# Kernel optimization log

Hardware: AMD Instinct MI355X
Metric: run time of the kernel (lower is better)

## Reference

```python
import jax, jax.numpy as jnp
import numpy as np

N_NODES = 50000
N_EDGES = 800000
IN_DIM, FEAT_DIM, HID_DIM, OUT_DIM = 512, 256, 256, 128


def _glorot(key, shape):
    fan_in = shape[-1]
    bound = 1.0 / np.sqrt(fan_in)
    return jax.random.uniform(key, shape, jnp.float32, -bound, bound)


def setup_inputs() -> dict:
    key = jax.random.key(0)
    ks = jax.random.split(key, 12)
    x = jax.random.normal(ks[0], (N_NODES, IN_DIM), jnp.float32)
    edge_index = jax.random.randint(ks[1], (2, N_EDGES), 0, N_NODES, jnp.int64)
    return {
        "x": x,
        "edge_index": edge_index,
        # feature_pre MLP
        "W_pre": _glorot(ks[2], (FEAT_DIM, IN_DIM)),
        "b_pre": jnp.zeros((FEAT_DIM,), jnp.float32),
        "W_pre2": _glorot(ks[3], (HID_DIM, FEAT_DIM)),
        "b_pre2": jnp.zeros((HID_DIM,), jnp.float32),
        # conv_first: SAGEConv(hidden, hidden); lin_l (neighbors, with bias), lin_r (root, no bias)
        "Wl1": _glorot(ks[4], (HID_DIM, HID_DIM)),
        "bl1": jnp.zeros((HID_DIM,), jnp.float32),
        "Wr1": _glorot(ks[5], (HID_DIM, HID_DIM)),
        # conv_out: SAGEConv(hidden, output)
        "Wl2": _glorot(ks[6], (OUT_DIM, HID_DIM)),
        "bl2": jnp.zeros((OUT_DIM,), jnp.float32),
        "Wr2": _glorot(ks[7], (OUT_DIM, HID_DIM)),
    }


def sage_conv(x, src, dst, Wl, bl, Wr):
    # mean-aggregate source features at destination nodes, then linear + root linear
    n = x.shape[0]
    msg = x[src]                                               # [E, D]
    agg = jax.ops.segment_sum(msg, dst, num_segments=n)        # [N, D]
    cnt = jax.ops.segment_sum(jnp.ones((src.shape[0],), x.dtype), dst, num_segments=n)
    mean = agg / jnp.maximum(cnt, 1.0)[:, None]
    return mean @ Wl.T + bl + x @ Wr.T


def reference(x, edge_index, W_pre, b_pre, W_pre2, b_pre2, Wl1, bl1, Wr1, Wl2, bl2, Wr2):
    src, dst = edge_index[0], edge_index[1]
    h = x @ W_pre.T + b_pre
    h = h @ W_pre2.T + b_pre2
    h = jax.nn.relu(sage_conv(h, src, dst, Wl1, bl1, Wr1))
    # dropout is identity in eval mode; layer_num=2 -> no hidden convs
    h = sage_conv(h, src, dst, Wl2, bl2, Wr2)
    # F.normalize(p=2, dim=-1), eps=1e-12
    norm = jnp.maximum(jnp.linalg.norm(h, axis=-1, keepdims=True), 1e-12)
    return h / norm
```

## Files before the change

kernel.cpp:

```cpp
#include <hip/hip_runtime.h>
#include <hip/hip_bf16.h>


typedef __attribute__((ext_vector_type(4))) float f32x4;
typedef __attribute__((ext_vector_type(8))) short s8v;

__device__ __forceinline__ float bf2f(unsigned short u) {
  union { unsigned int i; float f; } v; v.i = ((unsigned int)u) << 16; return v.f;
}
__device__ __forceinline__ unsigned short f2bf(float f) {
  unsigned int u = __builtin_bit_cast(unsigned int, f);
  u += 0x7fffu + ((u >> 16) & 1u);
  return (unsigned short)(u >> 16);
}

__global__ __launch_bounds__(256) void zero_int_kernel(int* __restrict__ p, int n) {
  int i = blockIdx.x * blockDim.x + threadIdx.x;
  const int stride = gridDim.x * blockDim.x;
  for (; i < n; i += stride) p[i] = 0;
}

__global__ __launch_bounds__(256) void count_kernel(const int* __restrict__ dst,
                                                    int* __restrict__ cnt, int E) {
  const int e = blockIdx.x * blockDim.x + threadIdx.x;
  if (e < E) atomicAdd(&cnt[dst[e]], 1);
}

__global__ __launch_bounds__(256) void scan_pass1(const int* __restrict__ cnt,
                                                  int* __restrict__ bsum, int M) {
  __shared__ int red[256];
  const int t = threadIdx.x;
  const int i = blockIdx.x * 256 + t;
  red[t] = (i < M) ? cnt[i] : 0;
  __syncthreads();
  for (int off = 128; off > 0; off >>= 1) {
    if (t < off) red[t] += red[t + off];
    __syncthreads();
  }
  if (t == 0) bsum[blockIdx.x] = red[0];
}

__global__ __launch_bounds__(256) void scan_pass2(const int* __restrict__ bsum,
    int* __restrict__ boff, int* __restrict__ rowptr, int nb, int M, int E) {
  __shared__ int buf[256];
  const int t = threadIdx.x;
  const int v = (t < nb) ? bsum[t] : 0;
  buf[t] = v;
  __syncthreads();
  for (int off = 1; off < 256; off <<= 1) {
    const int add = (t >= off) ? buf[t - off] : 0;
    __syncthreads();
    buf[t] += add;
    __syncthreads();
  }
  if (t < nb) boff[t] = buf[t] - v;
  if (t == 0) rowptr[M] = E;
}

__global__ __launch_bounds__(256) void scan_pass3(int* __restrict__ cnt,
    const int* __restrict__ boff, int* __restrict__ rowptr, int M) {
  __shared__ int buf[256];
  const int t = threadIdx.x;
  const int i = blockIdx.x * 256 + t;
  const int v = (i < M) ? cnt[i] : 0;
  buf[t] = v;
  __syncthreads();
  for (int off = 1; off < 256; off <<= 1) {
    const int add = (t >= off) ? buf[t - off] : 0;
    __syncthreads();
    buf[t] += add;
    __syncthreads();
  }
  if (i < M) {
    rowptr[i] = buf[t] - v + boff[blockIdx.x];
    cnt[i] = 0;
  }
}

__global__ __launch_bounds__(256) void fill_kernel(const int* __restrict__ src,
    const int* __restrict__ dst, const int* __restrict__ rowptr,
    int* __restrict__ cursor, unsigned short* __restrict__ eidx, int E) {
  const int e = blockIdx.x * blockDim.x + threadIdx.x;
  if (e >= E) return;
  const int d = dst[e];
  const int pos = rowptr[d] + atomicAdd(&cursor[d], 1);
  eidx[pos] = (unsigned short)src[e];
}

__global__ __launch_bounds__(256) void cvt_x_kernel(const float* __restrict__ x,
    unsigned short* __restrict__ xb, int n) {
  int i = (blockIdx.x * 256 + threadIdx.x) * 8;
  const int stride = gridDim.x * 256 * 8;
  for (; i < n; i += stride) {
    const float4 f0 = *(const float4*)(x + i);
    const float4 f1 = *(const float4*)(x + i + 4);
    s8v p;
    p[0] = (short)f2bf(f0.x); p[1] = (short)f2bf(f0.y);
    p[2] = (short)f2bf(f0.z); p[3] = (short)f2bf(f0.w);
    p[4] = (short)f2bf(f1.x); p[5] = (short)f2bf(f1.y);
    p[6] = (short)f2bf(f1.z); p[7] = (short)f2bf(f1.w);
    *(s8v*)(xb + i) = p;
  }
}

__global__ __launch_bounds__(256) void prep_kernel(const float* __restrict__ Wp,
    const float* __restrict__ Wp2, const float* __restrict__ bp,
    const float* __restrict__ bp2, const float* __restrict__ Wl1,
    const float* __restrict__ Wr1, const float* __restrict__ Wl2,
    const float* __restrict__ Wr2, unsigned short* __restrict__ Wc,
    float* __restrict__ bc, unsigned short* __restrict__ Bc1,
    unsigned short* __restrict__ Bc2) {
  const int b = blockIdx.x, t = threadIdx.x;
  if (b < 256) {
    __shared__ float wrow[256];
    wrow[t] = Wp2[b * 256 + t];
    __syncthreads();
    float a0 = 0.f, a1 = 0.f;
    for (int m = 0; m < 256; ++m) {
      const float w = wrow[m];
      a0 = fmaf(w, Wp[m * 512 + t], a0);
      a1 = fmaf(w, Wp[m * 512 + 256 + t], a1);
    }
    Wc[b * 512 + t] = f2bf(a0);
    Wc[b * 512 + 256 + t] = f2bf(a1);
  } else if (b == 256) {
    float s = 0.f;
    for (int m = 0; m < 256; ++m) s = fmaf(Wp2[t * 256 + m], bp[m], s);
    bc[t] = s + bp2[t];
  } else if (b < 769) {
    const int idx = (b - 257) * 256 + t;
    const int o = idx >> 9, k = idx & 511;
    const float v = (k < 256) ? Wl1[o * 256 + k] : Wr1[o * 256 + (k - 256)];
    Bc1[idx] = f2bf(v);
  } else {
    const int idx = (b - 769) * 256 + t;
    const int r = idx >> 8, k = idx & 255;
    const float v = (r < 128) ? Wl2[r * 256 + k] : Wr2[(r - 128) * 256 + k];
    Bc2[idx] = f2bf(v);
  }
}

template <int K, int ASTRIDE, int CSTRIDE, int CBASE, bool BIAS_EN, bool RELU_EN>
__global__ __launch_bounds__(256) void mfma_gemm(
    const unsigned short* __restrict__ Ap, const unsigned short* __restrict__ Bp,
    const float* __restrict__ bias, unsigned short* __restrict__ Cp, int M, int nwg) {
  constexpr int NT = K / 32;
  constexpr int BUF = 16384;
  __shared__ __align__(16) char smem[3 * BUF];

  const int xcd = blockIdx.x & 7, bidx = blockIdx.x >> 3;
  const int q = nwg >> 3, r = nwg & 7;
  const int wg = (xcd < r ? xcd * (q + 1) : r * (q + 1) + (xcd - r) * q) + bidx;
  const int bm = (wg >> 1) * 128;
  const int bn = (wg & 1) * 128;

  const int t = threadIdx.x, w = t >> 6, l = t & 63;
  const int wr = (w >> 1) * 64, wc = (w & 1) * 64;
  const int lane15 = l & 15, half = l >> 4;

  const int sr = t >> 2, sp = t & 3;
  const int ar0 = min(bm + sr, M - 1);
  const int ar1 = min(bm + 64 + sr, M - 1);
  const int sl0 = sp ^ ((sr >> 1) & 3);
  const int sl1 = sp ^ (((64 + sr) >> 1) & 3);
  const unsigned short* apb0 = Ap + (size_t)ar0 * ASTRIDE + sl0 * 8;
  const unsigned short* apb1 = Ap + (size_t)ar1 * ASTRIDE + sl1 * 8;
  const unsigned short* bpb0 = Bp + (size_t)(bn + sr) * K + sl0 * 8;
  const unsigned short* bpb1 = Bp + (size_t)(bn + 64 + sr) * K + sl1 * 8;

  f32x4 acc[4][4];
#pragma unroll
  for (int i = 0; i < 4; ++i)
#pragma unroll
    for (int j = 0; j < 4; ++j) acc[i][j] = f32x4{0.f, 0.f, 0.f, 0.f};

  auto stage = [&](int bufOff, int k0) {
    __builtin_amdgcn_global_load_lds((const unsigned int*)(apb0 + k0),
        (unsigned int*)(smem + bufOff + w * 1024), 16, 0, 0);
    __builtin_amdgcn_global_load_lds((const unsigned int*)(apb1 + k0),
        (unsigned int*)(smem + bufOff + 4096 + w * 1024), 16, 0, 0);
    __builtin_amdgcn_global_load_lds((const unsigned int*)(bpb0 + k0),
        (unsigned int*)(smem + bufOff + 8192 + w * 1024), 16, 0, 0);
    __builtin_amdgcn_global_load_lds((const unsigned int*)(bpb1 + k0),
        (unsigned int*)(smem + bufOff + 12288 + w * 1024), 16, 0, 0);
  };
  auto compute = [&](int bufOff) {
    const char* Ab = smem + bufOff;
    const char* Bb = Ab + 8192;
    s8v af[4], bv[4];
#pragma unroll
    for (int ms = 0; ms < 4; ++ms) {
      const int rr = wr + ms * 16 + lane15;
      af[ms] = *(const s8v*)(Ab + rr * 64 + ((half ^ ((rr >> 1) & 3)) << 4));
    }
#pragma unroll
    for (int ns = 0; ns < 4; ++ns) {
      const int rr = wc + ns * 16 + lane15;
      bv[ns] = *(const s8v*)(Bb + rr * 64 + ((half ^ ((rr >> 1) & 3)) << 4));
    }
#pragma unroll
    for (int ms = 0; ms < 4; ++ms)
#pragma unroll
      for (int ns = 0; ns < 4; ++ns)
        acc[ms][ns] =
            __builtin_amdgcn_mfma_f32_16x16x32_bf16(af[ms], bv[ns], acc[ms][ns], 0, 0, 0);
  };

  stage(0, 0);
  stage(BUF, 32);

  int offC = 0, offI = 2 * BUF;
#pragma unroll 1
  for (int tt = 0; tt < NT - 1; ++tt) {
    asm volatile("s_waitcnt vmcnt(4)" ::: "memory");
    __builtin_amdgcn_sched_barrier(0);
    __builtin_amdgcn_s_barrier();
    if (tt + 2 < NT) stage(offI, (tt + 2) * 32);
    compute(offC);
    offC = (offC == 2 * BUF) ? 0 : offC + BUF;
    offI = (offI == 2 * BUF) ? 0 : offI + BUF;
  }
  asm volatile("s_waitcnt vmcnt(0)" ::: "memory");
  __builtin_amdgcn_sched_barrier(0);
  __builtin_amdgcn_s_barrier();
  compute(offC);

  float bias_l[4];
  if (BIAS_EN) {
#pragma unroll
    for (int ns = 0; ns < 4; ++ns) bias_l[ns] = bias[bn + wc + ns * 16 + lane15];
  }
  constexpr int PITCH = 288;
#pragma unroll
  for (int pp = 0; pp < 2; ++pp) {
    __syncthreads();
#pragma unroll
    for (int mi = 0; mi < 2; ++mi) {
      const int ms = 2 * pp + mi;
      const int lrow0 = (wr >> 1) + (mi << 4) + half * 4;
#pragma unroll
      for (int ns = 0; ns < 4; ++ns) {
        f32x4 v = acc[ms][ns];
        if (BIAS_EN) {
#pragma unroll
          for (int rg = 0; rg < 4; ++rg) v[rg] += bias_l[ns];
        }
        if (RELU_EN) {
#pragma unroll
          for (int rg = 0; rg < 4; ++rg) v[rg] = fmaxf(v[rg], 0.f);
        }
        const int colb = (wc + ns * 16 + lane15) * 2;
#pragma unroll
        for (int rg = 0; rg < 4; ++rg)
          *(unsigned short*)(smem + (lrow0 + rg) * PITCH + colb) = f2bf(v[rg]);
      }
    }
    __syncthreads();
#pragma unroll
    for (int jj = 0; jj < 4; ++jj) {
      const int lr = jj * 16 + (t >> 4);
      const int wrg = (lr >= 32) ? 64 : 0;
      const int msg = 2 * pp + ((lr >> 4) & 1);
      const int grow = bm + wrg + msg * 16 + (lr & 15);
      if (grow < M) {
        const s8v val = *(const s8v*)(smem + lr * PITCH + lane15 * 16);
        *(s8v*)(Cp + (size_t)grow * CSTRIDE + CBASE + bn + lane15 * 8) = val;
      }
    }
  }
}

__global__ __launch_bounds__(256) void gather_mean256_kernel(
    unsigned short* __restrict__ Acat, const int* __restrict__ rowptr,
    const unsigned short* __restrict__ eidx, int M) {
  const int node = blockIdx.x * 4 + (threadIdx.x >> 6);
  if (node >= M) return;
  const int lane = threadIdx.x & 63;
  const int c4 = lane * 4;
  const int beg = rowptr[node], end = rowptr[node + 1];
  float a0 = 0.f, a1 = 0.f, a2 = 0.f, a3 = 0.f;
  int j = beg;
  for (; j + 3 < end; j += 4) {
    const size_t s0 = eidx[j], s1 = eidx[j + 1], s2 = eidx[j + 2], s3 = eidx[j + 3];
    const ushort4 v0 = *(const ushort4*)(Acat + s0 * 512 + 256 + c4);
    const ushort4 v1 = *(const ushort4*)(Acat + s1 * 512 + 256 + c4);
    const ushort4 v2 = *(const ushort4*)(Acat + s2 * 512 + 256 + c4);
    const ushort4 v3 = *(const ushort4*)(Acat + s3 * 512 + 256 + c4);
    a0 += (bf2f(v0.x) + bf2f(v1.x)) + (bf2f(v2.x) + bf2f(v3.x));
    a1 += (bf2f(v0.y) + bf2f(v1.y)) + (bf2f(v2.y) + bf2f(v3.y));
    a2 += (bf2f(v0.z) + bf2f(v1.z)) + (bf2f(v2.z) + bf2f(v3.z));
    a3 += (bf2f(v0.w) + bf2f(v1.w)) + (bf2f(v2.w) + bf2f(v3.w));
  }
  for (; j < end; ++j) {
    const size_t s0 = eidx[j];
    const ushort4 v0 = *(const ushort4*)(Acat + s0 * 512 + 256 + c4);
    a0 += bf2f(v0.x); a1 += bf2f(v0.y); a2 += bf2f(v0.z); a3 += bf2f(v0.w);
  }
  const float inv = 1.0f / fmaxf((float)(end - beg), 1.0f);
  ushort4 o;
  o.x = f2bf(a0 * inv); o.y = f2bf(a1 * inv);
  o.z = f2bf(a2 * inv); o.w = f2bf(a3 * inv);
  *(ushort4*)(Acat + (size_t)node * 512 + c4) = o;
}

__global__ __launch_bounds__(256) void gather_finalize_kernel(
    const unsigned short* __restrict__ Acat, const int* __restrict__ rowptr,
    const unsigned short* __restrict__ eidx, const float* __restrict__ bl2,
    float* __restrict__ out, int M) {
  const int node = blockIdx.x * 4 + (threadIdx.x >> 6);
  if (node >= M) return;
  const int lane = threadIdx.x & 63;
  const int c2 = lane * 2;
  const int beg = rowptr[node], end = rowptr[node + 1];
  float ax = 0.f, ay = 0.f;
  int j = beg;
  for (; j + 3 < end; j += 4) {
    const size_t s0 = eidx[j], s1 = eidx[j + 1], s2 = eidx[j + 2], s3 = eidx[j + 3];
    const ushort2 v0 = *(const ushort2*)(Acat + s0 * 512 + 256 + c2);
    const ushort2 v1 = *(const ushort2*)(Acat + s1 * 512 + 256 + c2);
    const ushort2 v2 = *(const ushort2*)(Acat + s2 * 512 + 256 + c2);
    const ushort2 v3 = *(const ushort2*)(Acat + s3 * 512 + 256 + c2);
    ax += (bf2f(v0.x) + bf2f(v1.x)) + (bf2f(v2.x) + bf2f(v3.x));
    ay += (bf2f(v0.y) + bf2f(v1.y)) + (bf2f(v2.y) + bf2f(v3.y));
  }
  for (; j < end; ++j) {
    const size_t s0 = eidx[j];
    const ushort2 v0 = *(const ushort2*)(Acat + s0 * 512 + 256 + c2);
    ax += bf2f(v0.x); ay += bf2f(v0.y);
  }
  const float inv = 1.0f / fmaxf((float)(end - beg), 1.0f);
  const ushort2 rr = *(const ushort2*)(Acat + (size_t)node * 512 + 384 + c2);
  const float2 b = *(const float2*)&bl2[c2];
  const float vx = fmaf(ax, inv, b.x) + bf2f(rr.x);
  const float vy = fmaf(ay, inv, b.y) + bf2f(rr.y);
  float ss = vx * vx + vy * vy;
#pragma unroll
  for (int off = 32; off > 0; off >>= 1) ss += __shfl_xor(ss, off);
  const float rn = 1.0f / fmaxf(sqrtf(ss), 1e-12f);
  *(float2*)&out[(size_t)node * 128 + c2] = make_float2(vx * rn, vy * rn);
}

extern "C" void kernel_launch(void* const* d_in, const int* in_sizes, int n_in,
                              void* d_out, int out_size, void* d_ws, size_t ws_size,
                              hipStream_t stream) {
  const float* x      = (const float*)d_in[0];
  const int*   ei     = (const int*)d_in[1];
  const float* W_pre  = (const float*)d_in[2];
  const float* b_pre  = (const float*)d_in[3];
  const float* W_pre2 = (const float*)d_in[4];
  const float* b_pre2 = (const float*)d_in[5];
  const float* Wl1    = (const float*)d_in[6];
  const float* bl1    = (const float*)d_in[7];
  const float* Wr1    = (const float*)d_in[8];
  const float* Wl2    = (const float*)d_in[9];
  const float* bl2    = (const float*)d_in[10];
  const float* Wr2    = (const float*)d_in[11];
  float* out = (float*)d_out;

  const int M = in_sizes[0] / 512;
  const int E = in_sizes[1] / 2;
  const int* src = ei;
  const int* dst = ei + E;

  char* p = (char*)d_ws;
  unsigned short* Acat = (unsigned short*)p; p += (size_t)M * 512 * 2;
  unsigned short* H3   = (unsigned short*)p; p += (size_t)M * 256 * 2;
  unsigned short* xb   = (unsigned short*)p; p += (size_t)M * 512 * 2;
  unsigned short* Wc   = (unsigned short*)p; p += 256 * 512 * 2;
  unsigned short* Bc1  = (unsigned short*)p; p += 256 * 512 * 2;
  unsigned short* Bc2  = (unsigned short*)p; p += 256 * 256 * 2;
  float* bc   = (float*)p; p += 256 * 4;
  int* rowptr = (int*)p;   p += (size_t)(M + 1) * 4;
  int* cnt    = (int*)p;   p += (size_t)M * 4;
  int* bsum   = (int*)p;   p += 256 * 4;
  int* boff   = (int*)p;   p += 256 * 4;
  unsigned short* eidx = (unsigned short*)p;

  const int eblk = (E + 255) / 256;
  const int nb   = (M + 255) / 256;
  const int nwg  = ((M + 127) / 128) * 2;
  const int nblk = (M + 3) / 4;

  cvt_x_kernel<<<2048, 256, 0, stream>>>(x, xb, M * 512);

  zero_int_kernel<<<256, 256, 0, stream>>>(cnt, M);
  count_kernel<<<eblk, 256, 0, stream>>>(dst, cnt, E);
  scan_pass1<<<nb, 256, 0, stream>>>(cnt, bsum, M);
  scan_pass2<<<1, 256, 0, stream>>>(bsum, boff, rowptr, nb, M, E);
  scan_pass3<<<nb, 256, 0, stream>>>(cnt, boff, rowptr, M);
  fill_kernel<<<eblk, 256, 0, stream>>>(src, dst, rowptr, cnt, eidx, E);

  prep_kernel<<<1025, 256, 0, stream>>>(W_pre, W_pre2, b_pre, b_pre2,
                                        Wl1, Wr1, Wl2, Wr2, Wc, bc, Bc1, Bc2);

  mfma_gemm<512, 512, 512, 256, true, false>
      <<<nwg, 256, 0, stream>>>(xb, Wc, bc, Acat, M, nwg);
  gather_mean256_kernel<<<nblk, 256, 0, stream>>>(Acat, rowptr, eidx, M);
  mfma_gemm<512, 512, 256, 0, true, true>
      <<<nwg, 256, 0, stream>>>(Acat, Bc1, bl1, H3, M, nwg);
  mfma_gemm<256, 256, 512, 256, false, false>
      <<<nwg, 256, 0, stream>>>(H3, Bc2, nullptr, Acat, M, nwg);
  gather_finalize_kernel<<<nblk, 256, 0, stream>>>(Acat, rowptr, eidx, bl2, out, M);
}
```

Measured before the change: 288.0 us.

## Fuse fp32-to-bf16 conversion of input into first GEMM's A-tile staging

Removes the separate conversion kernel and its bf16 workspace buffer; the first GEMM now loads fp32 rows of x into registers, converts them to bf16 and writes them into swizzled LDS. The B operand still uses direct global-to-LDS loads. This is meant to cut the extra memory round trip and one kernel launch. In exchange the GEMM reads twice as many bytes for A, including redundant reads across the two column-tile workgroups, and it adds register pressure and VALU conversion work inside the pipelined loop.

```diff
diff --git a/kernel.cpp b/kernel.cpp
--- a/kernel.cpp
+++ b/kernel.cpp
@@ -85,22 +85,6 @@
   const int d = dst[e];
   const int pos = rowptr[d] + atomicAdd(&cursor[d], 1);
   eidx[pos] = (unsigned short)src[e];
-}
-
-__global__ __launch_bounds__(256) void cvt_x_kernel(const float* __restrict__ x,
-    unsigned short* __restrict__ xb, int n) {
-  int i = (blockIdx.x * 256 + threadIdx.x) * 8;
-  const int stride = gridDim.x * 256 * 8;
-  for (; i < n; i += stride) {
-    const float4 f0 = *(const float4*)(x + i);
-    const float4 f1 = *(const float4*)(x + i + 4);
-    s8v p;
-    p[0] = (short)f2bf(f0.x); p[1] = (short)f2bf(f0.y);
-    p[2] = (short)f2bf(f0.z); p[3] = (short)f2bf(f0.w);
-    p[4] = (short)f2bf(f1.x); p[5] = (short)f2bf(f1.y);
-    p[6] = (short)f2bf(f1.z); p[7] = (short)f2bf(f1.w);
-    *(s8v*)(xb + i) = p;
-  }
 }
 
 __global__ __launch_bounds__(256) void prep_kernel(const float* __restrict__ Wp,
@@ -140,10 +124,10 @@
   }
 }
 
-template <int K, int ASTRIDE, int CSTRIDE, int CBASE, bool BIAS_EN, bool RELU_EN>
-__global__ __launch_bounds__(256) void mfma_gemm(
-    const unsigned short* __restrict__ Ap, const unsigned short* __restrict__ Bp,
-    const float* __restrict__ bias, unsigned short* __restrict__ Cp, int M, int nwg) {
+template <int K, int ASTRIDE, int CSTRIDE, int CBASE, bool BIAS_EN, bool RELU_EN, bool A_FP32>
+__global__ __launch_bounds__(256) void mfma_gemm(const void* __restrict__ Ap,
+    const unsigned short* __restrict__ Bp, const float* __restrict__ bias,
+    unsigned short* __restrict__ Cp, int M, int nwg) {
   constexpr int NT = K / 32;
   constexpr int BUF = 16384;
   __shared__ __align__(16) char smem[3 * BUF];
@@ -159,22 +143,26 @@
   const int lane15 = l & 15, half = l >> 4;
 
   const int sr = t >> 2, sp = t & 3;
-  const int ar0 = min(bm + sr, M - 1);
-  const int ar1 = min(bm + 64 + sr, M - 1);
   const int sl0 = sp ^ ((sr >> 1) & 3);
   const int sl1 = sp ^ (((64 + sr) >> 1) & 3);
-  const unsigned short* apb0 = Ap + (size_t)ar0 * ASTRIDE + sl0 * 8;
-  const unsigned short* apb1 = Ap + (size_t)ar1 * ASTRIDE + sl1 * 8;
+  const unsigned short* Abf = (const unsigned short*)Ap;
+  const unsigned short* apb0 = Abf + (size_t)min(bm + sr, M - 1) * ASTRIDE + sl0 * 8;
+  const unsigned short* apb1 = Abf + (size_t)min(bm + 64 + sr, M - 1) * ASTRIDE + sl1 * 8;
   const unsigned short* bpb0 = Bp + (size_t)(bn + sr) * K + sl0 * 8;
   const unsigned short* bpb1 = Bp + (size_t)(bn + 64 + sr) * K + sl1 * 8;
 
+  const int fr = t >> 1, fh = t & 1;
+  const float* Afp = (const float*)Ap + (size_t)min(bm + fr, M - 1) * ASTRIDE + fh * 16;
+  const int fs0 = (2 * fh + 0) ^ ((fr >> 1) & 3);
+  const int fs1 = (2 * fh + 1) ^ ((fr >> 1) & 3);
+
   f32x4 acc[4][4];
 #pragma unroll
   for (int i = 0; i < 4; ++i)
 #pragma unroll
     for (int j = 0; j < 4; ++j) acc[i][j] = f32x4{0.f, 0.f, 0.f, 0.f};
 
-  auto stage = [&](int bufOff, int k0) {
+  auto stageAll = [&](int bufOff, int k0) {
     __builtin_amdgcn_global_load_lds((const unsigned int*)(apb0 + k0),
         (unsigned int*)(smem + bufOff + w * 1024), 16, 0, 0);
     __builtin_amdgcn_global_load_lds((const unsigned int*)(apb1 + k0),
@@ -184,6 +172,31 @@
     __builtin_amdgcn_global_load_lds((const unsigned int*)(bpb1 + k0),
         (unsigned int*)(smem + bufOff + 12288 + w * 1024), 16, 0, 0);
   };
+  auto stageB2 = [&](int bufOff, int k0) {
+    __builtin_amdgcn_global_load_lds((const unsigned int*)(bpb0 + k0),
+        (unsigned int*)(smem + bufOff + 8192 + w * 1024), 16, 0, 0);
+    __builtin_amdgcn_global_load_lds((const unsigned int*)(bpb1 + k0),
+        (unsigned int*)(smem + bufOff + 12288 + w * 1024), 16, 0, 0);
+  };
+  auto loadA = [&](int k0, float4* ar) {
+    ar[0] = *(const float4*)(Afp + k0 + 0);
+    ar[1] = *(const float4*)(Afp + k0 + 4);
+    ar[2] = *(const float4*)(Afp + k0 + 8);
+    ar[3] = *(const float4*)(Afp + k0 + 12);
+  };
+  auto writeA = [&](int bufOff, const float4* ar) {
+    s8v p0, p1;
+    p0[0] = (short)f2bf(ar[0].x); p0[1] = (short)f2bf(ar[0].y);
+    p0[2] = (short)f2bf(ar[0].z); p0[3] = (short)f2bf(ar[0].w);
+    p0[4] = (short)f2bf(ar[1].x); p0[5] = (short)f2bf(ar[1].y);
+    p0[6] = (short)f2bf(ar[1].z); p0[7] = (short)f2bf(ar[1].w);
+    p1[0] = (short)f2bf(ar[2].x); p1[1] = (short)f2bf(ar[2].y);
+    p1[2] = (short)f2bf(ar[2].z); p1[3] = (short)f2bf(ar[2].w);
+    p1[4] = (short)f2bf(ar[3].x); p1[5] = (short)f2bf(ar[3].y);
+    p1[6] = (short)f2bf(ar[3].z); p1[7] = (short)f2bf(ar[3].w);
+    *(s8v*)(smem + bufOff + fr * 64 + fs0 * 16) = p0;
+    *(s8v*)(smem + bufOff + fr * 64 + fs1 * 16) = p1;
+  };
   auto compute = [&](int bufOff) {
     const char* Ab = smem + bufOff;
     const char* Bb = Ab + 8192;
@@ -206,24 +219,69 @@
             __builtin_amdgcn_mfma_f32_16x16x32_bf16(af[ms], bv[ns], acc[ms][ns], 0, 0, 0);
   };
 
-  stage(0, 0);
-  stage(BUF, 32);
-
-  int offC = 0, offI = 2 * BUF;
+  if constexpr (A_FP32) {
+    static_assert(NT % 2 == 0, "fp32 path assumes even NT");
+    float4 arE[4], arO[4];
+    loadA(0, arE);
+    __builtin_amdgcn_sched_barrier(0);
+    stageB2(0, 0);
+    __builtin_amdgcn_sched_barrier(0);
+    loadA(32, arO);
+    __builtin_amdgcn_sched_barrier(0);
+    stageB2(BUF, 32);
+    __builtin_amdgcn_sched_barrier(0);
+    writeA(0, arE);
+
+    auto iterF = [&](int tt, int ofC, int ofW, int ofI,
+                     float4 (&arW)[4], float4 (&arI)[4]) {
+      asm volatile("s_waitcnt vmcnt(2)" ::: "memory");
+      __builtin_amdgcn_sched_barrier(0);
+      writeA(ofW, arW);
+      asm volatile("s_waitcnt lgkmcnt(0)" ::: "memory");
+      __builtin_amdgcn_sched_barrier(0);
+      __builtin_amdgcn_s_barrier();
+      if (tt + 2 < NT) {
+        loadA((tt + 2) * 32, arI);
+        __builtin_amdgcn_sched_barrier(0);
+        stageB2(ofI, (tt + 2) * 32);
+        __builtin_amdgcn_sched_barrier(0);
+      }
+      compute(ofC);
+    };
+    auto rot = [](int o) { return o == 2 * BUF ? 0 : o + BUF; };
+    int ofC = 0, ofW = BUF, ofI = 2 * BUF;
 #pragma unroll 1
-  for (int tt = 0; tt < NT - 1; ++tt) {
-    asm volatile("s_waitcnt vmcnt(4)" ::: "memory");
+    for (int tt = 0; tt + 1 < NT - 1; tt += 2) {
+      iterF(tt, ofC, ofW, ofI, arO, arE);
+      ofC = rot(ofC); ofW = rot(ofW); ofI = rot(ofI);
+      iterF(tt + 1, ofC, ofW, ofI, arE, arO);
+      ofC = rot(ofC); ofW = rot(ofW); ofI = rot(ofI);
+    }
+    iterF(NT - 2, ofC, ofW, ofI, arO, arE);
+    ofC = rot(ofC);
+    asm volatile("s_waitcnt vmcnt(0)" ::: "memory");
     __builtin_amdgcn_sched_barrier(0);
     __builtin_amdgcn_s_barrier();
-    if (tt + 2 < NT) stage(offI, (tt + 2) * 32);
+    compute(ofC);
+  } else {
+    stageAll(0, 0);
+    stageAll(BUF, 32);
+    int offC = 0, offI = 2 * BUF;
+#pragma unroll 1
+    for (int tt = 0; tt < NT - 1; ++tt) {
+      asm volatile("s_waitcnt vmcnt(4)" ::: "memory");
+      __builtin_amdgcn_sched_barrier(0);
+      __builtin_amdgcn_s_barrier();
+      if (tt + 2 < NT) stageAll(offI, (tt + 2) * 32);
+      compute(offC);
+      offC = (offC == 2 * BUF) ? 0 : offC + BUF;
+      offI = (offI == 2 * BUF) ? 0 : offI + BUF;
+    }
+    asm volatile("s_waitcnt vmcnt(0)" ::: "memory");
+    __builtin_amdgcn_sched_barrier(0);
+    __builtin_amdgcn_s_barrier();
     compute(offC);
-    offC = (offC == 2 * BUF) ? 0 : offC + BUF;
-    offI = (offI == 2 * BUF) ? 0 : offI + BUF;
-  }
-  asm volatile("s_waitcnt vmcnt(0)" ::: "memory");
-  __builtin_amdgcn_sched_barrier(0);
-  __builtin_amdgcn_s_barrier();
-  compute(offC);
+  }
 
   float bias_l[4];
   if (BIAS_EN) {
@@ -365,7 +423,6 @@
   char* p = (char*)d_ws;
   unsigned short* Acat = (unsigned short*)p; p += (size_t)M * 512 * 2;
   unsigned short* H3   = (unsigned short*)p; p += (size_t)M * 256 * 2;
-  unsigned short* xb   = (unsigned short*)p; p += (size_t)M * 512 * 2;
   unsigned short* Wc   = (unsigned short*)p; p += 256 * 512 * 2;
   unsigned short* Bc1  = (unsigned short*)p; p += 256 * 512 * 2;
   unsigned short* Bc2  = (unsigned short*)p; p += 256 * 256 * 2;
@@ -381,8 +438,6 @@
   const int nwg  = ((M + 127) / 128) * 2;
   const int nblk = (M + 3) / 4;
 
-  cvt_x_kernel<<<2048, 256, 0, stream>>>(x, xb, M * 512);
-
   zero_int_kernel<<<256, 256, 0, stream>>>(cnt, M);
   count_kernel<<<eblk, 256, 0, stream>>>(dst, cnt, E);
   scan_pass1<<<nb, 256, 0, stream>>>(cnt, bsum, M);
@@ -393,12 +448,12 @@
   prep_kernel<<<1025, 256, 0, stream>>>(W_pre, W_pre2, b_pre, b_pre2,
                                         Wl1, Wr1, Wl2, Wr2, Wc, bc, Bc1, Bc2);
 
-  mfma_gemm<512, 512, 512, 256, true, false>
-      <<<nwg, 256, 0, stream>>>(xb, Wc, bc, Acat, M, nwg);
+  mfma_gemm<512, 512, 512, 256, true, false, true>
+      <<<nwg, 256, 0, stream>>>(x, Wc, bc, Acat, M, nwg);
   gather_mean256_kernel<<<nblk, 256, 0, stream>>>(Acat, rowptr, eidx, M);
-  mfma_gemm<512, 512, 256, 0, true, true>
+  mfma_gemm<512, 512, 256, 0, true, true, false>
       <<<nwg, 256, 0, stream>>>(Acat, Bc1, bl1, H3, M, nwg);
-  mfma_gemm<256, 256, 512, 256, false, false>
+  mfma_gemm<256, 256, 512, 256, false, false, false>
       <<<nwg, 256, 0, stream>>>(H3, Bc2, nullptr, Acat, M, nwg);
   gather_finalize_kernel<<<nblk, 256, 0, stream>>>(Acat, rowptr, eidx, bl2, out, M);
 }
```

Result: faster. 276.7 us (-3.9%).
